# Optimization experiments

Hardware: AMD Instinct MI355X
Metric: run time of the kernel (lower is better)

## Reference

```python
import jax, jax.numpy as jnp
import numpy as np

N_GT = 8192
N_PRED = 8192
DIM = 3
EDGE_PROB = 6.0 / N_PRED  # sparse mesh-like adjacency, avg degree ~6


def setup_inputs() -> dict:
    key = jax.random.key(0)
    k1, k2, k3, k4 = jax.random.split(key, 4)
    preds = jax.random.normal(k1, (N_PRED, DIM), dtype=jnp.float32)
    gts = jax.random.normal(k2, (N_GT, DIM), dtype=jnp.float32)
    gts_normals = jax.random.normal(k3, (N_GT, DIM), dtype=jnp.float32)
    # binary float adjacency matrix, as in the torch module (A cast to FloatTensor)
    A = (jax.random.uniform(k4, (N_PRED, N_PRED)) < EDGE_PROB).astype(jnp.float32)
    return {"preds": preds, "gts": gts, "gts_normals": gts_normals, "A": A}


def reference(preds, gts, gts_normals, A):
    # --- batch_pairwise_dist(gts, preds): P[i, j] = ||gts_i - preds_j||^2 ---
    # (N_gt, N_pred); computed via the same rx + ry - 2*zz expansion
    P = (
        jnp.sum(gts * gts, axis=1)[:, None]
        + jnp.sum(preds * preds, axis=1)[None, :]
        - 2.0 * gts @ preds.T
    )
    nearest_gt = jnp.argmin(P, axis=0)          # (N_pred,) index into gts
    q = gts_normals[nearest_gt]                  # (N_pred, 3) nearest-neighbor normals

    # --- normal_pred + calculate_loss, fused ---
    # Original builds x_diff[d, i, j] = (preds[i, d] - preds[j, d]) * A[i, j]
    # then inner[i, j] = sum_d q[j, d] * x_diff[d, i, j], loss = sum(inner^2).
    # Equivalent without the (3, N, N) tensor:
    #   dot[i, j] = preds[i] . q[j] - preds[j] . q[j]
    dot = preds @ q.T - jnp.sum(preds * q, axis=1)[None, :]  # (N_pred, N_pred)
    inner = dot * A
    return jnp.sum(inner * inner)
```

## Files before the change

### kernel.cpp

```cpp
#include <hip/hip_runtime.h>

#define N 8192
#define NNB 512
#define SCB 1536
#define GRID_B (NNB + SCB)
#define CQUADS 512
#define NCHUNKS (N * (N / 4) / CQUADS)
#define NN_CH 13
#define SC_CH 17
#define SLOT_CAP 256
#define GCHUNK 1024

static_assert(NNB * NN_CH + SCB * SC_CH == NCHUNKS, "chunk split must cover A");


__global__ __launch_bounds__(256) void fused_kernel(
        const float* __restrict__ preds,
        const float* __restrict__ gts,
        const float* __restrict__ gn,
        float4* __restrict__ qpq,
        const float4* __restrict__ A4,
        unsigned int* __restrict__ cnt,
        uint2* __restrict__ hits,
        float* __restrict__ out) {
    __shared__ __align__(16) float sgf[GCHUNK * 3];
    __shared__ unsigned int scnt;

    const int tid = threadIdx.x;
    const int b   = blockIdx.x;

    int ch0, nch;
    if (b < NNB) {
        if (b == 0 && tid == 0) out[0] = 0.0f;

        const int lane = tid & 63;
        const int wv   = tid >> 6;
        const int j0   = b * 16 + wv * 4;

        float px[4], py[4], pz[4], bestV[4];
        int bestI[4];
        #pragma unroll
        for (int k = 0; k < 4; ++k) {
            px[k] = preds[(j0 + k) * 3 + 0];
            py[k] = preds[(j0 + k) * 3 + 1];
            pz[k] = preds[(j0 + k) * 3 + 2];
            bestV[k] = 3.4e38f;
            bestI[k] = 0;
        }

        for (int c = 0; c < N / GCHUNK; ++c) {
            #pragma unroll
            for (int s = 0; s < GCHUNK * 3 / 256; ++s) {
                const int t = s * 256 + tid;
                sgf[t] = gts[c * GCHUNK * 3 + t];
            }
            __syncthreads();

            #pragma unroll 4
            for (int it = 0; it < GCHUNK / 64; ++it) {
                const int t  = it * 64 + lane;
                const float gx = sgf[t * 3 + 0];
                const float gy = sgf[t * 3 + 1];
                const float gz = sgf[t * 3 + 2];
                float gg = gx * gx;
                gg = fmaf(gy, gy, gg);
                gg = fmaf(gz, gz, gg);
                const int gi = c * GCHUNK + t;
                #pragma unroll
                for (int k = 0; k < 4; ++k) {
                    float d = gx * px[k];
                    d = fmaf(gy, py[k], d);
                    d = fmaf(gz, pz[k], d);
                    const float v = fmaf(-2.0f, d, gg);
                    if (v < bestV[k]) { bestV[k] = v; bestI[k] = gi; }
                }
            }
            __syncthreads();
        }

        #pragma unroll
        for (int d = 1; d < 64; d <<= 1) {
            #pragma unroll
            for (int k = 0; k < 4; ++k) {
                const float ov = __shfl_xor(bestV[k], d);
                const int   oi = __shfl_xor(bestI[k], d);
                if (ov < bestV[k] || (ov == bestV[k] && oi < bestI[k])) {
                    bestV[k] = ov; bestI[k] = oi;
                }
            }
        }

        if (lane == 0) {
            #pragma unroll
            for (int k = 0; k < 4; ++k) {
                const int bi = bestI[k];
                const float qx = gn[bi * 3 + 0];
                const float qy = gn[bi * 3 + 1];
                const float qz = gn[bi * 3 + 2];
                const float pq = px[k] * qx + py[k] * qy + pz[k] * qz;
                qpq[j0 + k] = make_float4(qx, qy, qz, pq);
            }
        }

        ch0 = b * NN_CH;
        nch = NN_CH;
    } else {
        ch0 = NNB * NN_CH + (b - NNB) * SC_CH;
        nch = SC_CH;
    }

    if (tid == 0) scnt = 0u;
    __syncthreads();

    uint2* hbuf = (uint2*)sgf;
    uint2* slot = hits + (size_t)b * SLOT_CAP;

    for (int cc = 0; cc < nch; ++cc) {
        const int base = (ch0 + cc) * CQUADS + tid;
        const float4 a0 = A4[base];
        const float4 a1 = A4[base + 256];

        #pragma unroll
        for (int h = 0; h < 2; ++h) {
            const float4 a = h ? a1 : a0;
            const int u = h ? (base + 256) : base;
            if (a.x != 0.0f || a.y != 0.0f || a.z != 0.0f || a.w != 0.0f) {
                const unsigned int i  = (unsigned)(u >> 11);
                const unsigned int j0 = (unsigned)((u & 2047) << 2);
                const float av[4] = { a.x, a.y, a.z, a.w };
                #pragma unroll
                for (int c = 0; c < 4; ++c) {
                    if (av[c] != 0.0f) {
                        const unsigned int p = atomicAdd(&scnt, 1u);
                        if (p < SLOT_CAP) {
                            hbuf[p] = make_uint2((i << 13) | (j0 + c),
                                                 __float_as_uint(av[c]));
                        }
                    }
                }
            }
        }
    }

    __syncthreads();
    const unsigned int n = scnt < SLOT_CAP ? scnt : SLOT_CAP;
    for (unsigned int t = tid; t < n; t += 256) slot[t] = hbuf[t];
    if (tid == 0) cnt[b] = n;
}

__global__ __launch_bounds__(256) void loss_kernel(
        const float* __restrict__ preds,
        const float4* __restrict__ qpq,
        const unsigned int* __restrict__ cnt,
        const uint2* __restrict__ hits,
        float* __restrict__ out) {
    const int lane    = threadIdx.x & 63;
    const int wave_id = blockIdx.x * 4 + (threadIdx.x >> 6);
    float sum = 0.0f;

    #pragma unroll
    for (int s = 0; s < 4; ++s) {
        const int sb = wave_id * 4 + s;
        const unsigned int c = cnt[sb] < SLOT_CAP ? cnt[sb] : SLOT_CAP;
        const uint2* slot = hits + (size_t)sb * SLOT_CAP;
        for (unsigned int t = lane; t < c; t += 64) {
            const uint2 h = slot[t];
            const unsigned int i = h.x >> 13;
            const unsigned int j = h.x & 8191u;
            const float av = __uint_as_float(h.y);
            const float4 q = qpq[j];
            float d = preds[i * 3 + 0] * q.x;
            d = fmaf(preds[i * 3 + 1], q.y, d);
            d = fmaf(preds[i * 3 + 2], q.z, d);
            d = (d - q.w) * av;
            sum = fmaf(d, d, sum);
        }
    }

    #pragma unroll
    for (int d = 32; d > 0; d >>= 1) sum += __shfl_down(sum, d);

    __shared__ float wsum[4];
    if (lane == 0) wsum[threadIdx.x >> 6] = sum;
    __syncthreads();
    if (threadIdx.x == 0) {
        atomicAdd(out, wsum[0] + wsum[1] + wsum[2] + wsum[3]);
    }
}

extern "C" void kernel_launch(void* const* d_in, const int* in_sizes, int n_in,
                              void* d_out, int out_size, void* d_ws, size_t ws_size,
                              hipStream_t stream) {
    const float* preds = (const float*)d_in[0];
    const float* gts   = (const float*)d_in[1];
    const float* gn    = (const float*)d_in[2];
    const float* A     = (const float*)d_in[3];
    float* out = (float*)d_out;

    char* ws = (char*)d_ws;
    float4*       qpq  = (float4*)(ws);
    unsigned int* cnt  = (unsigned int*)(ws + 131072);
    uint2*        hits = (uint2*)(ws + 139264);

    fused_kernel<<<GRID_B, 256, 0, stream>>>(
        preds, gts, gn, qpq, (const float4*)A, cnt, hits, out);
    loss_kernel<<<128, 256, 0, stream>>>(preds, qpq, cnt, hits, out);
}
```

Measured before the change: 50.05 us.

## Make all blocks uniform, interleaving nearest-neighbor search with adjacency scan

Before, 512 blocks did the nearest-neighbor search and 1536 blocks only scanned A. Now every one of the 2048 blocks handles 4 predictions and 16 chunks of A. The gts chunk loads are interleaved with the A loads so the memory stream overlaps the distance compute. The 4 waves split the gts points and a cross-wave shared-memory reduction picks the argmin, which balances the load across blocks. It also adds an occupancy hint via launch bounds and a separate shared buffer for hits. Each block now re-reads all of gts, which raises L2 traffic.

```diff
diff --git a/kernel.cpp b/kernel.cpp
--- a/kernel.cpp
+++ b/kernel.cpp
@@ -1,20 +1,16 @@
 #include <hip/hip_runtime.h>
 
 #define N 8192
-#define NNB 512
-#define SCB 1536
-#define GRID_B (NNB + SCB)
+#define GRID_B 2048
 #define CQUADS 512
-#define NCHUNKS (N * (N / 4) / CQUADS)
-#define NN_CH 13
-#define SC_CH 17
+#define CPB 16
+#define GCH 1024
+#define NGCH (N / GCH)
+#define PPB 4
 #define SLOT_CAP 256
-#define GCHUNK 1024
-
-static_assert(NNB * NN_CH + SCB * SC_CH == NCHUNKS, "chunk split must cover A");
-
-
-__global__ __launch_bounds__(256) void fused_kernel(
+
+
+__global__ __launch_bounds__(256, 8) void fused_kernel(
         const float* __restrict__ preds,
         const float* __restrict__ gts,
         const float* __restrict__ gn,
@@ -23,51 +19,60 @@
         unsigned int* __restrict__ cnt,
         uint2* __restrict__ hits,
         float* __restrict__ out) {
-    __shared__ __align__(16) float sgf[GCHUNK * 3];
+    __shared__ __align__(16) float sgf[GCH * 3];
+    __shared__ uint2 hbuf[SLOT_CAP];
     __shared__ unsigned int scnt;
-
-    const int tid = threadIdx.x;
-    const int b   = blockIdx.x;
-
-    int ch0, nch;
-    if (b < NNB) {
-        if (b == 0 && tid == 0) out[0] = 0.0f;
-
-        const int lane = tid & 63;
-        const int wv   = tid >> 6;
-        const int j0   = b * 16 + wv * 4;
-
-        float px[4], py[4], pz[4], bestV[4];
-        int bestI[4];
-        #pragma unroll
-        for (int k = 0; k < 4; ++k) {
-            px[k] = preds[(j0 + k) * 3 + 0];
-            py[k] = preds[(j0 + k) * 3 + 1];
-            pz[k] = preds[(j0 + k) * 3 + 2];
-            bestV[k] = 3.4e38f;
-            bestI[k] = 0;
-        }
-
-        for (int c = 0; c < N / GCHUNK; ++c) {
+    __shared__ float swV[4][PPB];
+    __shared__ int   swI[4][PPB];
+
+    const int tid  = threadIdx.x;
+    const int b    = blockIdx.x;
+    const int lane = tid & 63;
+    const int wv   = tid >> 6;
+    const int j0   = b * PPB;
+
+    if (b == 0 && tid == 0) out[0] = 0.0f;
+
+    float px[PPB], py[PPB], pz[PPB], bestV[PPB];
+    int bestI[PPB];
+    #pragma unroll
+    for (int k = 0; k < PPB; ++k) {
+        px[k] = preds[(j0 + k) * 3 + 0];
+        py[k] = preds[(j0 + k) * 3 + 1];
+        pz[k] = preds[(j0 + k) * 3 + 2];
+        bestV[k] = 3.4e38f;
+        bestI[k] = 0;
+    }
+    if (tid == 0) scnt = 0u;
+
+    for (int c = 0; c < CPB; ++c) {
+        const int base = (b * CPB + c) * CQUADS + tid;
+        const float4 a0 = A4[base];
+        const float4 a1 = A4[base + 256];
+
+        if (c < NGCH) {
+            const float4* g4 = (const float4*)gts + (size_t)c * (GCH * 3 / 4);
+            const float4 t0 = g4[tid];
+            const float4 t1 = g4[tid + 256];
+            const float4 t2 = g4[tid + 512];
+            float4* s4 = (float4*)sgf;
+            s4[tid]       = t0;
+            s4[tid + 256] = t1;
+            s4[tid + 512] = t2;
+            __syncthreads();
+
             #pragma unroll
-            for (int s = 0; s < GCHUNK * 3 / 256; ++s) {
-                const int t = s * 256 + tid;
-                sgf[t] = gts[c * GCHUNK * 3 + t];
-            }
-            __syncthreads();
-
-            #pragma unroll 4
-            for (int it = 0; it < GCHUNK / 64; ++it) {
-                const int t  = it * 64 + lane;
+            for (int m = 0; m < 4; ++m) {
+                const int t  = wv * 256 + m * 64 + lane;
                 const float gx = sgf[t * 3 + 0];
                 const float gy = sgf[t * 3 + 1];
                 const float gz = sgf[t * 3 + 2];
                 float gg = gx * gx;
                 gg = fmaf(gy, gy, gg);
                 gg = fmaf(gz, gz, gg);
-                const int gi = c * GCHUNK + t;
+                const int gi = c * GCH + t;
                 #pragma unroll
-                for (int k = 0; k < 4; ++k) {
+                for (int k = 0; k < PPB; ++k) {
                     float d = gx * px[k];
                     d = fmaf(gy, py[k], d);
                     d = fmaf(gz, pz[k], d);
@@ -75,50 +80,7 @@
                     if (v < bestV[k]) { bestV[k] = v; bestI[k] = gi; }
                 }
             }
-            __syncthreads();
-        }
-
-        #pragma unroll
-        for (int d = 1; d < 64; d <<= 1) {
-            #pragma unroll
-            for (int k = 0; k < 4; ++k) {
-                const float ov = __shfl_xor(bestV[k], d);
-                const int   oi = __shfl_xor(bestI[k], d);
-                if (ov < bestV[k] || (ov == bestV[k] && oi < bestI[k])) {
-                    bestV[k] = ov; bestI[k] = oi;
-                }
-            }
-        }
-
-        if (lane == 0) {
-            #pragma unroll
-            for (int k = 0; k < 4; ++k) {
-                const int bi = bestI[k];
-                const float qx = gn[bi * 3 + 0];
-                const float qy = gn[bi * 3 + 1];
-                const float qz = gn[bi * 3 + 2];
-                const float pq = px[k] * qx + py[k] * qy + pz[k] * qz;
-                qpq[j0 + k] = make_float4(qx, qy, qz, pq);
-            }
-        }
-
-        ch0 = b * NN_CH;
-        nch = NN_CH;
-    } else {
-        ch0 = NNB * NN_CH + (b - NNB) * SC_CH;
-        nch = SC_CH;
-    }
-
-    if (tid == 0) scnt = 0u;
-    __syncthreads();
-
-    uint2* hbuf = (uint2*)sgf;
-    uint2* slot = hits + (size_t)b * SLOT_CAP;
-
-    for (int cc = 0; cc < nch; ++cc) {
-        const int base = (ch0 + cc) * CQUADS + tid;
-        const float4 a0 = A4[base];
-        const float4 a1 = A4[base + 256];
+        }
 
         #pragma unroll
         for (int h = 0; h < 2; ++h) {
@@ -126,24 +88,62 @@
             const int u = h ? (base + 256) : base;
             if (a.x != 0.0f || a.y != 0.0f || a.z != 0.0f || a.w != 0.0f) {
                 const unsigned int i  = (unsigned)(u >> 11);
-                const unsigned int j0 = (unsigned)((u & 2047) << 2);
+                const unsigned int jq = (unsigned)((u & 2047) << 2);
                 const float av[4] = { a.x, a.y, a.z, a.w };
                 #pragma unroll
-                for (int c = 0; c < 4; ++c) {
-                    if (av[c] != 0.0f) {
+                for (int e = 0; e < 4; ++e) {
+                    if (av[e] != 0.0f) {
                         const unsigned int p = atomicAdd(&scnt, 1u);
                         if (p < SLOT_CAP) {
-                            hbuf[p] = make_uint2((i << 13) | (j0 + c),
-                                                 __float_as_uint(av[c]));
+                            hbuf[p] = make_uint2((i << 13) | (jq + e),
+                                                 __float_as_uint(av[e]));
                         }
                     }
                 }
             }
         }
-    }
-
+
+        if (c < NGCH) __syncthreads();
+    }
+
+    #pragma unroll
+    for (int d = 1; d < 64; d <<= 1) {
+        #pragma unroll
+        for (int k = 0; k < PPB; ++k) {
+            const float ov = __shfl_xor(bestV[k], d);
+            const int   oi = __shfl_xor(bestI[k], d);
+            if (ov < bestV[k] || (ov == bestV[k] && oi < bestI[k])) {
+                bestV[k] = ov; bestI[k] = oi;
+            }
+        }
+    }
+    if (lane == 0) {
+        #pragma unroll
+        for (int k = 0; k < PPB; ++k) { swV[wv][k] = bestV[k]; swI[wv][k] = bestI[k]; }
+    }
     __syncthreads();
+
+    if (tid < PPB) {
+        float bv = swV[0][tid];
+        int   bi = swI[0][tid];
+        #pragma unroll
+        for (int w = 1; w < 4; ++w) {
+            const float v = swV[w][tid];
+            const int   i = swI[w][tid];
+            if (v < bv || (v == bv && i < bi)) { bv = v; bi = i; }
+        }
+        const float qx = gn[bi * 3 + 0];
+        const float qy = gn[bi * 3 + 1];
+        const float qz = gn[bi * 3 + 2];
+        const float ppx = preds[(j0 + tid) * 3 + 0];
+        const float ppy = preds[(j0 + tid) * 3 + 1];
+        const float ppz = preds[(j0 + tid) * 3 + 2];
+        const float pq = ppx * qx + ppy * qy + ppz * qz;
+        qpq[j0 + tid] = make_float4(qx, qy, qz, pq);
+    }
+
     const unsigned int n = scnt < SLOT_CAP ? scnt : SLOT_CAP;
+    uint2* slot = hits + (size_t)b * SLOT_CAP;
     for (unsigned int t = tid; t < n; t += 256) slot[t] = hbuf[t];
     if (tid == 0) cnt[b] = n;
 }
```

New measurement: 54.33 us. 8.6% more time.
